# Kernel optimization log

Measured on AMD Instinct MI355X. Metric: run time of the kernel, lower is better.

## Reference

```python
import jax, jax.numpy as jnp
import numpy as np

B, T, C, H = 4, 2048, 2048, 16
HD = C // H  # head_dim = 128


def setup_inputs() -> dict:
    key = jax.random.key(0)
    k1, k2, k3 = jax.random.split(key, 3)
    x = jax.random.normal(k1, (B, T, C), dtype=jnp.float32)
    w_qkv = jax.random.normal(k2, (C, 3 * C), dtype=jnp.float32) * (C ** -0.5)
    w_proj = jax.random.normal(k3, (C, C), dtype=jnp.float32) * (C ** -0.5)
    return {"x": x, "w_qkv": w_qkv, "w_proj": w_proj}


def reference(x, w_qkv, w_proj):
    Bx, Tx, Cx = x.shape
    qkv = x @ w_qkv                       # [B, T, 3C]
    q, k, v = jnp.split(qkv, 3, axis=-1)  # each [B, T, C]

    def split_heads(t):
        return t.reshape(Bx, Tx, H, HD).transpose(0, 2, 1, 3)  # [B, H, T, HD]

    q, k, v = split_heads(q), split_heads(k), split_heads(v)
    scale = HD ** -0.5
    attn = jnp.einsum("bhqd,bhkd->bhqk", q, k) * scale  # [B, H, T, T]
    causal = jnp.tril(jnp.ones((Tx, Tx), dtype=bool))
    attn = jnp.where(causal[None, None], attn, -jnp.inf)
    attn = jax.nn.softmax(attn, axis=-1)
    out = jnp.einsum("bhqk,bhkd->bhqd", attn, v)        # [B, H, T, HD]
    out = out.transpose(0, 2, 1, 3).reshape(Bx, Tx, Cx)  # [B, T, C]
    return out @ w_proj
```

## Files before the change

kernel.cpp:

```cpp
#include <hip/hip_runtime.h>
#include <hip/hip_bf16.h>
#include <math.h>

typedef __bf16 bf16;
typedef __bf16 bf16x8 __attribute__((ext_vector_type(8)));
typedef float f32x4 __attribute__((ext_vector_type(4)));

#define AS1(p) ((const __attribute__((address_space(1))) void*)(p))
#define AS3(p) ((__attribute__((address_space(3))) void*)(p))

__device__ __forceinline__ void gl_lds16(const bf16* g, bf16* l) {
    __builtin_amdgcn_global_load_lds(AS1(g), AS3(l), 16, 0, 0);
}

__global__ __launch_bounds__(256) void cast_f32_bf16(const float* __restrict__ in,
                                                     bf16* __restrict__ out, long n) {
    long i = ((long)blockIdx.x * 256 + threadIdx.x) * 4;
    if (i + 3 < n) {
        float4 v = *(const float4*)(in + i);
        out[i + 0] = (bf16)v.x;
        out[i + 1] = (bf16)v.y;
        out[i + 2] = (bf16)v.z;
        out[i + 3] = (bf16)v.w;
    }
}

__global__ __launch_bounds__(256) void transpose_cast(const float* __restrict__ in,
                                                      bf16* __restrict__ out,
                                                      int R, int Cc) {
    __shared__ float tile[32][33];
    const int t = threadIdx.x;
    const int r0 = blockIdx.y * 32, c0 = blockIdx.x * 32;
    for (int i = 0; i < 4; ++i) {
        int idx = t + i * 256;
        int r = idx >> 5, c = idx & 31;
        tile[r][c] = in[(size_t)(r0 + r) * Cc + c0 + c];
    }
    __syncthreads();
    for (int i = 0; i < 4; ++i) {
        int idx = t + i * 256;
        int r = idx >> 5, c = idx & 31;
        out[(size_t)(c0 + r) * R + r0 + c] = (bf16)tile[c][r];
    }
}

template <typename OT>
__global__ __launch_bounds__(512, 2) void gemm256_bt(const bf16* __restrict__ A,
                                                     const bf16* __restrict__ BT,
                                                     OT* __restrict__ C,
                                                     int M, int N, int K) {
    __shared__ bf16 lds[2][2][256 * 64];
    const int t = threadIdx.x;
    const int lane = t & 63;
    const int w = t >> 6;
    const int wr = w >> 2, wc = w & 3;
    const int l15 = lane & 15, lg = lane >> 4;

    const int nbx = gridDim.x, nby = gridDim.y;
    const int orig = blockIdx.y * nbx + blockIdx.x;
    const int span = nby * 8;
    const int grp = orig / span, rem = orig % span;
    const int bm = rem >> 3, bn = grp * 8 + (rem & 7);

    const bf16* Ab = A + (size_t)bm * 256 * K;
    const bf16* Bb = BT + (size_t)bn * 256 * K;

    f32x4 acc[8][4] = {};

    const int nk = K / 64;
    int cur = 0;
    for (int j = 0; j < 4; ++j) {
        int cid = j * 512 + t;
        int r = cid >> 3, c = cid & 7;
        int src = (c ^ (r & 7)) << 3;
        gl_lds16(Ab + (size_t)r * K + src, &lds[0][0][cid * 8]);
        gl_lds16(Bb + (size_t)r * K + src, &lds[0][1][cid * 8]);
    }

    for (int kt = 0; kt < nk; ++kt) {
        __syncthreads();

        if (kt + 1 < nk) {
            const int k0 = (kt + 1) * 64;
            for (int j = 0; j < 4; ++j) {
                int cid = j * 512 + t;
                int r = cid >> 3, c = cid & 7;
                int src = (c ^ (r & 7)) << 3;
                gl_lds16(Ab + (size_t)r * K + k0 + src, &lds[cur ^ 1][0][cid * 8]);
                gl_lds16(Bb + (size_t)r * K + k0 + src, &lds[cur ^ 1][1][cid * 8]);
            }
        }

        const bf16* lA = &lds[cur][0][0];
        const bf16* lB = &lds[cur][1][0];
        bf16x8 bfrag[2][4];
        for (int kk = 0; kk < 2; ++kk)
            for (int n = 0; n < 4; ++n) {
                int R = wc * 64 + n * 16 + l15;
                bfrag[kk][n] = *(const bf16x8*)(lB + R * 64 + (((kk * 4 + lg) ^ (R & 7)) << 3));
            }
        __builtin_amdgcn_s_setprio(1);
        for (int m = 0; m < 8; ++m) {
            int R = wr * 128 + m * 16 + l15;
            bf16x8 a0 = *(const bf16x8*)(lA + R * 64 + ((lg ^ (R & 7)) << 3));
            bf16x8 a1 = *(const bf16x8*)(lA + R * 64 + (((4 + lg) ^ (R & 7)) << 3));
            for (int n = 0; n < 4; ++n) {
                acc[m][n] = __builtin_amdgcn_mfma_f32_16x16x32_bf16(a0, bfrag[0][n], acc[m][n], 0, 0, 0);
                acc[m][n] = __builtin_amdgcn_mfma_f32_16x16x32_bf16(a1, bfrag[1][n], acc[m][n], 0, 0, 0);
            }
        }
        __builtin_amdgcn_s_setprio(0);
        cur ^= 1;
    }

    for (int m = 0; m < 8; ++m)
        for (int n = 0; n < 4; ++n) {
            int row = bm * 256 + wr * 128 + m * 16 + lg * 4;
            int col = bn * 256 + wc * 64 + n * 16 + l15;
            for (int r = 0; r < 4; ++r)
                C[(size_t)(row + r) * N + col] = (OT)acc[m][n][r];
        }
}

__global__ __launch_bounds__(256, 2) void attn_fwd(const bf16* __restrict__ QKV,
                                                   bf16* __restrict__ O) {
    __shared__ bf16 lK[64 * 128];
    __shared__ bf16 lVt[128 * 64];
    __shared__ bf16 lP[4][32 * 68];

    const int t = threadIdx.x, lane = t & 63, w = t >> 6;
    const int l15 = lane & 15, lg = lane >> 4;
    const int bh = blockIdx.y;
    const int b = bh >> 4, h = bh & 15;
    const size_t rs = 6144;

    const bf16* Qb = QKV + (size_t)b * 2048 * rs + h * 128;
    const bf16* Kb = Qb + 2048;
    const bf16* Vb = Qb + 4096;

    const float C = 0.12751705f;
    const int kvp = t & 31;
    const int hd0 = (t >> 5) * 16;

    for (int half = 0; half < 2; ++half) {
        const int qt = half == 0 ? (15 - (int)blockIdx.x) : (int)blockIdx.x;
        const int q0 = qt * 128;
        const int qa = q0 + w * 32;

        bf16x8 qf[2][4];
        for (int f = 0; f < 2; ++f)
            for (int kk = 0; kk < 4; ++kk)
                qf[f][kk] = *(const bf16x8*)(Qb + (size_t)(qa + f * 16 + l15) * rs + kk * 32 + lg * 8);

        f32x4 o[2][8] = {};
        float m2[2][4], l2[2][4];
        for (int f = 0; f < 2; ++f)
            for (int r = 0; r < 4; ++r) { m2[f][r] = -1e30f; l2[f][r] = 0.f; }

        const int nt = q0 / 64 + 2;

        for (int j = 0; j < 4; ++j) {
            int c = j * 256 + t;
            int r = c >> 4, cc = c & 15;
            gl_lds16(Kb + (size_t)r * rs + ((cc ^ (r & 7)) << 3), lK + (size_t)c * 8);
        }
        bf16x8 vr0, vr1, vr2, vr3;
        {
            const bf16* p = Vb + (size_t)(2 * kvp) * rs + hd0;
            vr0 = *(const bf16x8*)(p);
            vr1 = *(const bf16x8*)(p + rs);
            vr2 = *(const bf16x8*)(p + 8);
            vr3 = *(const bf16x8*)(p + rs + 8);
        }

        for (int kt = 0; kt < nt; ++kt) {
            const int kv0 = kt * 64;
            __syncthreads();

            for (int e = 0; e < 8; ++e) {
                union { bf16 h2[2]; unsigned u; } p0, p1;
                p0.h2[0] = vr0[e]; p0.h2[1] = vr1[e];
                p1.h2[0] = vr2[e]; p1.h2[1] = vr3[e];
                int r0 = hd0 + e, r1 = hd0 + 8 + e;
                *(unsigned*)(lVt + r0 * 64 + (((kvp >> 2) ^ (r0 & 7)) << 3) + ((kvp & 3) << 1)) = p0.u;
                *(unsigned*)(lVt + r1 * 64 + (((kvp >> 2) ^ (r1 & 7)) << 3) + ((kvp & 3) << 1)) = p1.u;
            }

            f32x4 s[2][4] = {};
            __builtin_amdgcn_s_setprio(1);
            for (int n = 0; n < 4; ++n) {
                int row = n * 16 + l15;
                for (int kk = 0; kk < 4; ++kk) {
                    bf16x8 kf = *(const bf16x8*)(lK + row * 128 + (((kk * 4 + lg) ^ (row & 7)) << 3));
                    s[0][n] = __builtin_amdgcn_mfma_f32_16x16x32_bf16(qf[0][kk], kf, s[0][n], 0, 0, 0);
                    s[1][n] = __builtin_amdgcn_mfma_f32_16x16x32_bf16(qf[1][kk], kf, s[1][n], 0, 0, 0);
                }
            }
            __builtin_amdgcn_s_setprio(0);

            float pv[2][4][4];
            for (int f = 0; f < 2; ++f)
                for (int n = 0; n < 4; ++n)
                    for (int r = 0; r < 4; ++r) {
                        float x = s[f][n][r] * C;
                        int qg = qa + f * 16 + lg * 4 + r;
                        int kg = kv0 + n * 16 + l15;
                        pv[f][n][r] = (kg <= qg) ? x : -1e30f;
                    }
            float pmax[2][4];
            for (int f = 0; f < 2; ++f)
                for (int r = 0; r < 4; ++r)
                    pmax[f][r] = fmaxf(fmaxf(pv[f][0][r], pv[f][1][r]), fmaxf(pv[f][2][r], pv[f][3][r]));
            for (int d = 1; d < 16; d <<= 1)
                for (int f = 0; f < 2; ++f)
                    for (int r = 0; r < 4; ++r)
                        pmax[f][r] = fmaxf(pmax[f][r], __shfl_xor(pmax[f][r], d));
            bool need = false;
            for (int f = 0; f < 2; ++f)
                for (int r = 0; r < 4; ++r)
                    need = need || (pmax[f][r] > m2[f][r] + 8.f);
            if (__any(need ? 1 : 0)) {
                for (int f = 0; f < 2; ++f)
                    for (int r = 0; r < 4; ++r) {
                        float mn = fmaxf(m2[f][r], pmax[f][r]);
                        float al = exp2f(m2[f][r] - mn);
                        m2[f][r] = mn;
                        l2[f][r] *= al;
                        for (int j = 0; j < 8; ++j) o[f][j][r] *= al;
                    }
            }
            for (int f = 0; f < 2; ++f)
                for (int n = 0; n < 4; ++n)
                    for (int r = 0; r < 4; ++r) {
                        float p = exp2f(pv[f][n][r] - m2[f][r]);
                        l2[f][r] += p;
                        lP[w][(f * 16 + lg * 4 + r) * 68 + n * 16 + l15] = (bf16)p;
                    }
            bf16x8 pf[2][2];
            for (int f = 0; f < 2; ++f) {
                pf[f][0] = *(const bf16x8*)(&lP[w][(f * 16 + l15) * 68 + lg * 8]);
                pf[f][1] = *(const bf16x8*)(&lP[w][(f * 16 + l15) * 68 + 32 + lg * 8]);
            }

            __syncthreads();

            if (kt + 1 < nt) {
                const int nk2 = kv0 + 64;
                for (int j = 0; j < 4; ++j) {
                    int c = j * 256 + t;
                    int r = c >> 4, cc = c & 15;
                    gl_lds16(Kb + (size_t)(nk2 + r) * rs + ((cc ^ (r & 7)) << 3), lK + (size_t)c * 8);
                }
                const bf16* p = Vb + (size_t)(nk2 + 2 * kvp) * rs + hd0;
                vr0 = *(const bf16x8*)(p);
                vr1 = *(const bf16x8*)(p + rs);
                vr2 = *(const bf16x8*)(p + 8);
                vr3 = *(const bf16x8*)(p + rs + 8);
            }

            __builtin_amdgcn_s_setprio(1);
            for (int j = 0; j < 8; ++j) {
                int R = j * 16 + l15;
                bf16x8 vfa = *(const bf16x8*)(lVt + R * 64 + ((lg ^ (R & 7)) << 3));
                bf16x8 vfb = *(const bf16x8*)(lVt + R * 64 + (((4 + lg) ^ (R & 7)) << 3));
                o[0][j] = __builtin_amdgcn_mfma_f32_16x16x32_bf16(pf[0][0], vfa, o[0][j], 0, 0, 0);
                o[0][j] = __builtin_amdgcn_mfma_f32_16x16x32_bf16(pf[0][1], vfb, o[0][j], 0, 0, 0);
                o[1][j] = __builtin_amdgcn_mfma_f32_16x16x32_bf16(pf[1][0], vfa, o[1][j], 0, 0, 0);
                o[1][j] = __builtin_amdgcn_mfma_f32_16x16x32_bf16(pf[1][1], vfb, o[1][j], 0, 0, 0);
            }
            __builtin_amdgcn_s_setprio(0);
        }

        for (int d = 1; d < 16; d <<= 1)
            for (int f = 0; f < 2; ++f)
                for (int r = 0; r < 4; ++r)
                    l2[f][r] += __shfl_xor(l2[f][r], d);
        for (int f = 0; f < 2; ++f) {
            float inv[4];
            for (int r = 0; r < 4; ++r) inv[r] = 1.f / l2[f][r];
            bf16* Ob = O + ((size_t)b * 2048 + qa + f * 16) * 2048 + h * 128;
            for (int j = 0; j < 8; ++j)
                for (int r = 0; r < 4; ++r)
                    Ob[(size_t)(lg * 4 + r) * 2048 + j * 16 + l15] = (bf16)(o[f][j][r] * inv[r]);
        }
    }
}

extern "C" void kernel_launch(void* const* d_in, const int* in_sizes, int n_in,
                              void* d_out, int out_size, void* d_ws, size_t ws_size,
                              hipStream_t stream) {
    const float* x     = (const float*)d_in[0];
    const float* wqkv  = (const float*)d_in[1];
    const float* wproj = (const float*)d_in[2];
    float* out = (float*)d_out;

    char* ws = (char*)d_ws;
    bf16* xb     = (bf16*)(ws);
    bf16* wqkvT  = (bf16*)(ws + 33554432);
    bf16* wprojT = (bf16*)(ws + 33554432 + 25165824);
    bf16* QKV    = (bf16*)(ws + 33554432 + 25165824 + 8388608);
    bf16* Obuf   = xb;

    cast_f32_bf16<<<dim3(16384), 256, 0, stream>>>(x, xb, (long)8192 * 2048);
    transpose_cast<<<dim3(192, 64), 256, 0, stream>>>(wqkv, wqkvT, 2048, 6144);
    transpose_cast<<<dim3(64, 64), 256, 0, stream>>>(wproj, wprojT, 2048, 2048);
    gemm256_bt<bf16><<<dim3(24, 32), 512, 0, stream>>>(xb, wqkvT, QKV, 8192, 6144, 2048);
    attn_fwd<<<dim3(8, 64), 256, 0, stream>>>(QKV, Obuf);
    gemm256_bt<float><<<dim3(8, 32), 512, 0, stream>>>(Obuf, wprojT, out, 8192, 2048, 2048);
}
```

Baseline: 459.7 us.

## Split GEMM k-tile into four phased MFMA clusters with interleaved prefetch

```diff
diff --git a/kernel.cpp b/kernel.cpp
--- a/kernel.cpp
+++ b/kernel.cpp
@@ -80,9 +80,13 @@
     for (int kt = 0; kt < nk; ++kt) {
         __syncthreads();
 
-        if (kt + 1 < nk) {
-            const int k0 = (kt + 1) * 64;
-            for (int j = 0; j < 4; ++j) {
+        const bf16* lA = &lds[cur][0][0];
+        const bf16* lB = &lds[cur][1][0];
+        const bool pf = (kt + 1 < nk);
+        const int k0 = (kt + 1) * 64;
+
+        if (pf) {
+            for (int j = 0; j < 2; ++j) {
                 int cid = j * 512 + t;
                 int r = cid >> 3, c = cid & 7;
                 int src = (c ^ (r & 7)) << 3;
@@ -90,26 +94,72 @@
                 gl_lds16(Bb + (size_t)r * K + k0 + src, &lds[cur ^ 1][1][cid * 8]);
             }
         }
-
-        const bf16* lA = &lds[cur][0][0];
-        const bf16* lB = &lds[cur][1][0];
-        bf16x8 bfrag[2][4];
-        for (int kk = 0; kk < 2; ++kk)
-            for (int n = 0; n < 4; ++n) {
-                int R = wc * 64 + n * 16 + l15;
-                bfrag[kk][n] = *(const bf16x8*)(lB + R * 64 + (((kk * 4 + lg) ^ (R & 7)) << 3));
-            }
+        bf16x8 bf0[4], am[4];
+        for (int n = 0; n < 4; ++n) {
+            int R = wc * 64 + n * 16 + l15;
+            bf0[n] = *(const bf16x8*)(lB + R * 64 + ((lg ^ (R & 7)) << 3));
+        }
+        for (int m = 0; m < 4; ++m) {
+            int R = wr * 128 + m * 16 + l15;
+            am[m] = *(const bf16x8*)(lA + R * 64 + ((lg ^ (R & 7)) << 3));
+        }
+        __builtin_amdgcn_s_barrier();
         __builtin_amdgcn_s_setprio(1);
-        for (int m = 0; m < 8; ++m) {
+        for (int m = 0; m < 4; ++m)
+            for (int n = 0; n < 4; ++n)
+                acc[m][n] = __builtin_amdgcn_mfma_f32_16x16x32_bf16(am[m], bf0[n], acc[m][n], 0, 0, 0);
+        __builtin_amdgcn_s_setprio(0);
+        __builtin_amdgcn_s_barrier();
+
+        if (pf) {
+            for (int j = 2; j < 4; ++j) {
+                int cid = j * 512 + t;
+                int r = cid >> 3, c = cid & 7;
+                int src = (c ^ (r & 7)) << 3;
+                gl_lds16(Ab + (size_t)r * K + k0 + src, &lds[cur ^ 1][0][cid * 8]);
+                gl_lds16(Bb + (size_t)r * K + k0 + src, &lds[cur ^ 1][1][cid * 8]);
+            }
+        }
+        for (int m = 0; m < 4; ++m) {
+            int R = wr * 128 + (m + 4) * 16 + l15;
+            am[m] = *(const bf16x8*)(lA + R * 64 + ((lg ^ (R & 7)) << 3));
+        }
+        __builtin_amdgcn_s_barrier();
+        __builtin_amdgcn_s_setprio(1);
+        for (int m = 0; m < 4; ++m)
+            for (int n = 0; n < 4; ++n)
+                acc[m + 4][n] = __builtin_amdgcn_mfma_f32_16x16x32_bf16(am[m], bf0[n], acc[m + 4][n], 0, 0, 0);
+        __builtin_amdgcn_s_setprio(0);
+        __builtin_amdgcn_s_barrier();
+
+        bf16x8 bf1[4];
+        for (int n = 0; n < 4; ++n) {
+            int R = wc * 64 + n * 16 + l15;
+            bf1[n] = *(const bf16x8*)(lB + R * 64 + (((4 + lg) ^ (R & 7)) << 3));
+        }
+        for (int m = 0; m < 4; ++m) {
             int R = wr * 128 + m * 16 + l15;
-            bf16x8 a0 = *(const bf16x8*)(lA + R * 64 + ((lg ^ (R & 7)) << 3));
-            bf16x8 a1 = *(const bf16x8*)(lA + R * 64 + (((4 + lg) ^ (R & 7)) << 3));
-            for (int n = 0; n < 4; ++n) {
-                acc[m][n] = __builtin_amdgcn_mfma_f32_16x16x32_bf16(a0, bfrag[0][n], acc[m][n], 0, 0, 0);
-                acc[m][n] = __builtin_amdgcn_mfma_f32_16x16x32_bf16(a1, bfrag[1][n], acc[m][n], 0, 0, 0);
-            }
-        }
+            am[m] = *(const bf16x8*)(lA + R * 64 + (((4 + lg) ^ (R & 7)) << 3));
+        }
+        __builtin_amdgcn_s_barrier();
+        __builtin_amdgcn_s_setprio(1);
+        for (int m = 0; m < 4; ++m)
+            for (int n = 0; n < 4; ++n)
+                acc[m][n] = __builtin_amdgcn_mfma_f32_16x16x32_bf16(am[m], bf1[n], acc[m][n], 0, 0, 0);
         __builtin_amdgcn_s_setprio(0);
+        __builtin_amdgcn_s_barrier();
+
+        for (int m = 0; m < 4; ++m) {
+            int R = wr * 128 + (m + 4) * 16 + l15;
+            am[m] = *(const bf16x8*)(lA + R * 64 + (((4 + lg) ^ (R & 7)) << 3));
+        }
+        __builtin_amdgcn_s_barrier();
+        __builtin_amdgcn_s_setprio(1);
+        for (int m = 0; m < 4; ++m)
+            for (int n = 0; n < 4; ++n)
+                acc[m + 4][n] = __builtin_amdgcn_mfma_f32_16x16x32_bf16(am[m], bf1[n], acc[m + 4][n], 0, 0, 0);
+        __builtin_amdgcn_s_setprio(0);
+
         cur ^= 1;
     }
 
```

New measurement: 464.6 us. No clear change (+1.1%).
